# Optimization experiments

Hardware: AMD Instinct MI355X
Metric: run time of the kernel (lower is better)

Reference implementation:

```python
import jax, jax.numpy as jnp
import numpy as np
from jax import lax

INPUT = 99
HIDDEN = 64
T = 65536


def setup_inputs() -> dict:
    key = jax.random.key(0)
    ks = jax.random.split(key, 8)
    x = jax.random.normal(ks[0], (1, T, INPUT), dtype=jnp.float32)
    # PyTorch LSTM params: weight_ih_l0 [4H, in], weight_hh_l0 [4H, H], biases [4H]
    s = 1.0 / np.sqrt(HIDDEN)
    W_ih = jax.random.uniform(ks[1], (4 * HIDDEN, INPUT), jnp.float32, -s, s)
    W_hh = jax.random.uniform(ks[2], (4 * HIDDEN, HIDDEN), jnp.float32, -s, s)
    b_ih = jax.random.uniform(ks[3], (4 * HIDDEN,), jnp.float32, -s, s)
    b_hh = jax.random.uniform(ks[4], (4 * HIDDEN,), jnp.float32, -s, s)
    # head: Linear(64->32, bias=False), Linear(32->3, bias=True)
    W1 = jax.random.normal(ks[5], (32, HIDDEN), dtype=jnp.float32) * 0.01
    W2 = jax.random.normal(ks[6], (3, 32), dtype=jnp.float32) * 0.01
    b2 = jnp.zeros((3,), dtype=jnp.float32)
    return {"x": x, "W_ih": W_ih, "W_hh": W_hh, "b_ih": b_ih, "b_hh": b_hh,
            "W1": W1, "W2": W2, "b2": b2}


def reference(x, W_ih, W_hh, b_ih, b_hh, W1, W2, b2):
    H = HIDDEN
    # Precompute input projections for all timesteps (one big GEMM).
    # x: [1, T, 99] -> xz: [T, 4H]; x[-1] == last (only) batch row.
    xz = jnp.einsum('td,gd->tg', x[-1], W_ih) + b_ih + b_hh

    def step(carry, z_t):
        h, c = carry
        z = z_t + W_hh @ h  # [4H]
        i, f, g, o = jnp.split(z, 4)  # PyTorch gate order: i, f, g, o
        i = jax.nn.sigmoid(i)
        f = jax.nn.sigmoid(f)
        g = jnp.tanh(g)
        o = jax.nn.sigmoid(o)
        c = f * c + i * g
        h = o * jnp.tanh(c)
        return (h, c), None

    h0 = jnp.zeros((H,), dtype=x.dtype)
    c0 = jnp.zeros((H,), dtype=x.dtype)
    (h_T, _), _ = lax.scan(step, (h0, c0), xz)

    # x[-1, -1] -> last timestep hidden of last batch row, then MLP head
    h = jax.nn.relu(h_T)
    h = jax.nn.relu(W1 @ h)
    out = W2 @ h + b2
    return out[None, :]  # [1, 3]
```

## Files before the change

kernel.cpp:

```cpp
#include <hip/hip_runtime.h>

#define T_STEPS 65536
#define NIN 99
#define HID 64
#define G4 256
#define TS 128
#define PF 8

typedef _Float16 half2v __attribute__((ext_vector_type(2)));

__device__ __forceinline__ float frcp(float x) { return __builtin_amdgcn_rcpf(x); }
__device__ __forceinline__ float fexp2(float x) { return __builtin_amdgcn_exp2f(x); }

#define LOG2E 1.4426950408889634f

__device__ __forceinline__ float sigmoid_f(float x) { return frcp(1.0f + fexp2(x * -LOG2E)); }
__device__ __forceinline__ float tanh_f(float x) {
    float ax = fabsf(x);
    float e  = fexp2(ax * (2.0f * LOG2E));
    float r  = 1.0f - 2.0f * frcp(e + 1.0f);
    return copysignf(r, x);
}

__device__ __forceinline__ half2v pk16(float a, float b) {
#if __has_builtin(__builtin_amdgcn_cvt_pkrtz)
    return __builtin_bit_cast(half2v, __builtin_amdgcn_cvt_pkrtz(a, b));
#else
    half2v r; r.x = (_Float16)a; r.y = (_Float16)b; return r;
#endif
}
__device__ __forceinline__ float fdot2f(half2v a, half2v b, float c) {
#if __has_builtin(__builtin_amdgcn_fdot2)
    return __builtin_amdgcn_fdot2(a, b, c, false);
#else
    return fmaf((float)a.x, (float)b.x, fmaf((float)a.y, (float)b.y, c));
#endif
}

#define BAR_LGKM() asm volatile("s_waitcnt lgkmcnt(0)\n\ts_barrier" ::: "memory")

__global__ __launch_bounds__(256, 1) void xz_kernel(
    const float* __restrict__ x, const float* __restrict__ W_ih,
    const float* __restrict__ b_ih, const float* __restrict__ b_hh,
    float* __restrict__ xz2) {
    __shared__ __align__(16) float xs[TS * 100];
    const int g  = threadIdx.x;
    const int t0 = blockIdx.x * TS;
    const int unit = g & 63, d = g >> 6;

    for (int i = g; i < TS * NIN; i += 256) {
        int tl = i / NIN;
        int j  = i - tl * NIN;
        xs[tl * 100 + j] = x[(size_t)t0 * NIN + i];
    }

    float w[NIN];
#pragma unroll
    for (int j = 0; j < NIN; ++j) w[j] = W_ih[g * NIN + j];
    const float bias = b_ih[g] + b_hh[g];
    __syncthreads();

    for (int tl = 0; tl < TS; ++tl) {
        const float* xr = &xs[tl * 100];
        float a0 = bias, a1 = 0.f, a2 = 0.f, a3 = 0.f;
#pragma unroll
        for (int j4 = 0; j4 < 24; ++j4) {
            float4 xv = *(const float4*)(xr + 4 * j4);
            a0 = fmaf(w[4 * j4 + 0], xv.x, a0);
            a1 = fmaf(w[4 * j4 + 1], xv.y, a1);
            a2 = fmaf(w[4 * j4 + 2], xv.z, a2);
            a3 = fmaf(w[4 * j4 + 3], xv.w, a3);
        }
        a0 = fmaf(w[96], xr[96], a0);
        a1 = fmaf(w[97], xr[97], a1);
        a2 = fmaf(w[98], xr[98], a2);
        xz2[(size_t)(t0 + tl) * G4 + unit * 4 + d] = (a0 + a1) + (a2 + a3);
    }
}

__global__ __launch_bounds__(256, 1) __attribute__((amdgpu_waves_per_eu(1)))
void lstm_kernel(
    const float* __restrict__ xz2, const float* __restrict__ W_hh,
    const float* __restrict__ W1, const float* __restrict__ W2,
    const float* __restrict__ b2, float* __restrict__ out) {
    __shared__ __align__(16) float4 pbuf[2][4][HID];
    __shared__ float hfin[HID];
    __shared__ float hbuf[32];
    const int tid = threadIdx.x;
    const int l   = tid & 63;
    const int wv  = tid >> 6;
    const int sb  = __builtin_amdgcn_readfirstlane(16 * wv);

    const float* Wb = W_hh + l * HID + sb;
    int wiP[8], wfP[8], wgP[8], woP[8];
#pragma unroll
    for (int j = 0; j < 8; ++j) {
        wiP[j] = __builtin_bit_cast(int, pk16(Wb[2 * j + 0],     Wb[2 * j + 1]));
        wfP[j] = __builtin_bit_cast(int, pk16(Wb[2 * j + 4096],  Wb[2 * j + 4097]));
        wgP[j] = __builtin_bit_cast(int, pk16(Wb[2 * j + 8192],  Wb[2 * j + 8193]));
        woP[j] = __builtin_bit_cast(int, pk16(Wb[2 * j + 12288], Wb[2 * j + 12289]));
        asm volatile("" : "+v"(wiP[j]), "+v"(wfP[j]), "+v"(wgP[j]), "+v"(woP[j]));
    }

    float h = 0.0f, c = 0.0f;

    const float* zi = xz2 + 4 * l;
    float4 zc0 = *(const float4*)(zi + (size_t)(wv)     * G4);
    float4 zc1 = *(const float4*)(zi + (size_t)(wv + 4) * G4);
    float4 zn0 = make_float4(0.f, 0.f, 0.f, 0.f);
    float4 zn1 = make_float4(0.f, 0.f, 0.f, 0.f);

    for (int tb = 0; tb < T_STEPS; tb += PF) {
        if (tb + PF < T_STEPS) {
            zn0 = *(const float4*)(zi + (size_t)(tb + PF + wv)     * G4);
            zn1 = *(const float4*)(zi + (size_t)(tb + PF + wv + 4) * G4);
        }
#pragma unroll
        for (int u = 0; u < PF; ++u) {
            const int par = u & 1;
            float ai, af, ag, ao;
            if (wv == (u & 3)) {
                float4 z = (u < 4) ? zc0 : zc1;
                ai = z.x; af = z.y; ag = z.z; ao = z.w;
            } else { ai = 0.f; af = 0.f; ag = 0.f; ao = 0.f; }

#if __has_builtin(__builtin_amdgcn_mov_dpp)
            float hn = __int_as_float(__builtin_amdgcn_mov_dpp(
                __float_as_int(h), 0xB1 , 0xF, 0xF, true));
#else
            float hn = __shfl_xor(h, 1, 64);
#endif
            const int hpi = __builtin_bit_cast(int, pk16(h, hn));
#pragma unroll
            for (int j = 0; j < 8; ++j) {
                half2v hpj = __builtin_bit_cast(half2v,
                    __builtin_amdgcn_readlane(hpi, sb + 2 * j));
                ai = fdot2f(__builtin_bit_cast(half2v, wiP[j]), hpj, ai);
                af = fdot2f(__builtin_bit_cast(half2v, wfP[j]), hpj, af);
                ag = fdot2f(__builtin_bit_cast(half2v, wgP[j]), hpj, ag);
                ao = fdot2f(__builtin_bit_cast(half2v, woP[j]), hpj, ao);
            }
            pbuf[par][wv][l] = make_float4(ai, af, ag, ao);
            BAR_LGKM();

            float4 r0 = pbuf[par][(wv + 1) & 3][l];
            float4 r1 = pbuf[par][(wv + 2) & 3][l];
            float4 r2 = pbuf[par][(wv + 3) & 3][l];
            float si = (ai + r0.x) + (r1.x + r2.x);
            float sf = (af + r0.y) + (r1.y + r2.y);
            float sg = (ag + r0.z) + (r1.z + r2.z);
            float so = (ao + r0.w) + (r1.w + r2.w);
            float ig = sigmoid_f(si);
            float fg = sigmoid_f(sf);
            float gg = tanh_f(sg);
            float og = sigmoid_f(so);
            c = fmaf(fg, c, ig * gg);
            h = og * tanh_f(c);
        }
        zc0 = zn0; zc1 = zn1;
    }

    if (tid < HID) hfin[tid] = h;
    __syncthreads();
    if (tid < 32) {
        float s = 0.0f;
#pragma unroll
        for (int j = 0; j < HID; ++j) s += W1[tid * HID + j] * fmaxf(hfin[j], 0.0f);
        hbuf[tid] = fmaxf(s, 0.0f);
    }
    __syncthreads();
    if (tid < 3) {
        float s = b2[tid];
#pragma unroll
        for (int j = 0; j < 32; ++j) s += W2[tid * 32 + j] * hbuf[j];
        out[tid] = s;
    }
}

extern "C" void kernel_launch(void* const* d_in, const int* in_sizes, int n_in,
                              void* d_out, int out_size, void* d_ws, size_t ws_size,
                              hipStream_t stream) {
    const float* x   = (const float*)d_in[0];
    const float* Wih = (const float*)d_in[1];
    const float* Whh = (const float*)d_in[2];
    const float* bih = (const float*)d_in[3];
    const float* bhh = (const float*)d_in[4];
    const float* W1  = (const float*)d_in[5];
    const float* W2  = (const float*)d_in[6];
    const float* b2  = (const float*)d_in[7];
    float* out = (float*)d_out;
    float* xz2 = (float*)d_ws;

    xz_kernel<<<T_STEPS / TS, 256, 0, stream>>>(x, Wih, bih, bhh, xz2);
    lstm_kernel<<<1, 256, 0, stream>>>(xz2, Whh, W1, W2, b2, out);
}
```

Measured before the change: 23.37 ms.

## Run LSTM recurrence in a single wavefront, removing LDS reduction and barriers

```diff
diff --git a/kernel.cpp b/kernel.cpp
--- a/kernel.cpp
+++ b/kernel.cpp
@@ -5,7 +5,7 @@
 #define HID 64
 #define G4 256
 #define TS 128
-#define PF 8
+#define PF 4
 
 typedef _Float16 half2v __attribute__((ext_vector_type(2)));
 
@@ -36,8 +36,6 @@
     return fmaf((float)a.x, (float)b.x, fmaf((float)a.y, (float)b.y, c));
 #endif
 }
-
-#define BAR_LGKM() asm volatile("s_waitcnt lgkmcnt(0)\n\ts_barrier" ::: "memory")
 
 __global__ __launch_bounds__(256, 1) void xz_kernel(
     const float* __restrict__ x, const float* __restrict__ W_ih,
@@ -78,23 +76,19 @@
     }
 }
 
-__global__ __launch_bounds__(256, 1) __attribute__((amdgpu_waves_per_eu(1)))
+__global__ __launch_bounds__(64, 1) __attribute__((amdgpu_waves_per_eu(1)))
 void lstm_kernel(
     const float* __restrict__ xz2, const float* __restrict__ W_hh,
     const float* __restrict__ W1, const float* __restrict__ W2,
     const float* __restrict__ b2, float* __restrict__ out) {
-    __shared__ __align__(16) float4 pbuf[2][4][HID];
     __shared__ float hfin[HID];
     __shared__ float hbuf[32];
-    const int tid = threadIdx.x;
-    const int l   = tid & 63;
-    const int wv  = tid >> 6;
-    const int sb  = __builtin_amdgcn_readfirstlane(16 * wv);
+    const int l = threadIdx.x;
 
-    const float* Wb = W_hh + l * HID + sb;
-    int wiP[8], wfP[8], wgP[8], woP[8];
+    const float* Wb = W_hh + l * HID;
+    int wiP[32], wfP[32], wgP[32], woP[32];
 #pragma unroll
-    for (int j = 0; j < 8; ++j) {
+    for (int j = 0; j < 32; ++j) {
         wiP[j] = __builtin_bit_cast(int, pk16(Wb[2 * j + 0],     Wb[2 * j + 1]));
         wfP[j] = __builtin_bit_cast(int, pk16(Wb[2 * j + 4096],  Wb[2 * j + 4097]));
         wgP[j] = __builtin_bit_cast(int, pk16(Wb[2 * j + 8192],  Wb[2 * j + 8193]));
@@ -105,24 +99,21 @@
     float h = 0.0f, c = 0.0f;
 
     const float* zi = xz2 + 4 * l;
-    float4 zc0 = *(const float4*)(zi + (size_t)(wv)     * G4);
-    float4 zc1 = *(const float4*)(zi + (size_t)(wv + 4) * G4);
-    float4 zn0 = make_float4(0.f, 0.f, 0.f, 0.f);
-    float4 zn1 = make_float4(0.f, 0.f, 0.f, 0.f);
+    float4 zcur[PF], znxt[PF];
+#pragma unroll
+    for (int p = 0; p < PF; ++p) zcur[p] = *(const float4*)(zi + (size_t)p * G4);
 
     for (int tb = 0; tb < T_STEPS; tb += PF) {
         if (tb + PF < T_STEPS) {
-            zn0 = *(const float4*)(zi + (size_t)(tb + PF + wv)     * G4);
-            zn1 = *(const float4*)(zi + (size_t)(tb + PF + wv + 4) * G4);
+#pragma unroll
+            for (int p = 0; p < PF; ++p)
+                znxt[p] = *(const float4*)(zi + (size_t)(tb + PF + p) * G4);
         }
 #pragma unroll
         for (int u = 0; u < PF; ++u) {
-            const int par = u & 1;
-            float ai, af, ag, ao;
-            if (wv == (u & 3)) {
-                float4 z = (u < 4) ? zc0 : zc1;
-                ai = z.x; af = z.y; ag = z.z; ao = z.w;
-            } else { ai = 0.f; af = 0.f; ag = 0.f; ao = 0.f; }
+            const float4 z = zcur[u];
+            float ai0 = z.x, af0 = z.y, ag0 = z.z, ao0 = z.w;
+            float ai1 = 0.f, af1 = 0.f, ag1 = 0.f, ao1 = 0.f;
 
 #if __has_builtin(__builtin_amdgcn_mov_dpp)
             float hn = __int_as_float(__builtin_amdgcn_mov_dpp(
@@ -132,24 +123,24 @@
 #endif
             const int hpi = __builtin_bit_cast(int, pk16(h, hn));
 #pragma unroll
-            for (int j = 0; j < 8; ++j) {
-                half2v hpj = __builtin_bit_cast(half2v,
-                    __builtin_amdgcn_readlane(hpi, sb + 2 * j));
-                ai = fdot2f(__builtin_bit_cast(half2v, wiP[j]), hpj, ai);
-                af = fdot2f(__builtin_bit_cast(half2v, wfP[j]), hpj, af);
-                ag = fdot2f(__builtin_bit_cast(half2v, wgP[j]), hpj, ag);
-                ao = fdot2f(__builtin_bit_cast(half2v, woP[j]), hpj, ao);
+            for (int j = 0; j < 16; ++j) {
+                half2v hp0 = __builtin_bit_cast(half2v,
+                    __builtin_amdgcn_readlane(hpi, 4 * j + 0));
+                half2v hp1 = __builtin_bit_cast(half2v,
+                    __builtin_amdgcn_readlane(hpi, 4 * j + 2));
+                ai0 = fdot2f(__builtin_bit_cast(half2v, wiP[2 * j]),     hp0, ai0);
+                af0 = fdot2f(__builtin_bit_cast(half2v, wfP[2 * j]),     hp0, af0);
+                ag0 = fdot2f(__builtin_bit_cast(half2v, wgP[2 * j]),     hp0, ag0);
+                ao0 = fdot2f(__builtin_bit_cast(half2v, woP[2 * j]),     hp0, ao0);
+                ai1 = fdot2f(__builtin_bit_cast(half2v, wiP[2 * j + 1]), hp1, ai1);
+                af1 = fdot2f(__builtin_bit_cast(half2v, wfP[2 * j + 1]), hp1, af1);
+                ag1 = fdot2f(__builtin_bit_cast(half2v, wgP[2 * j + 1]), hp1, ag1);
+                ao1 = fdot2f(__builtin_bit_cast(half2v, woP[2 * j + 1]), hp1, ao1);
             }
-            pbuf[par][wv][l] = make_float4(ai, af, ag, ao);
-            BAR_LGKM();
-
-            float4 r0 = pbuf[par][(wv + 1) & 3][l];
-            float4 r1 = pbuf[par][(wv + 2) & 3][l];
-            float4 r2 = pbuf[par][(wv + 3) & 3][l];
-            float si = (ai + r0.x) + (r1.x + r2.x);
-            float sf = (af + r0.y) + (r1.y + r2.y);
-            float sg = (ag + r0.z) + (r1.z + r2.z);
-            float so = (ao + r0.w) + (r1.w + r2.w);
+            float si = ai0 + ai1;
+            float sf = af0 + af1;
+            float sg = ag0 + ag1;
+            float so = ao0 + ao1;
             float ig = sigmoid_f(si);
             float fg = sigmoid_f(sf);
             float gg = tanh_f(sg);
@@ -157,23 +148,24 @@
             c = fmaf(fg, c, ig * gg);
             h = og * tanh_f(c);
         }
-        zc0 = zn0; zc1 = zn1;
+#pragma unroll
+        for (int p = 0; p < PF; ++p) zcur[p] = znxt[p];
     }
 
-    if (tid < HID) hfin[tid] = h;
+    hfin[l] = h;
     __syncthreads();
-    if (tid < 32) {
+    if (l < 32) {
         float s = 0.0f;
 #pragma unroll
-        for (int j = 0; j < HID; ++j) s += W1[tid * HID + j] * fmaxf(hfin[j], 0.0f);
-        hbuf[tid] = fmaxf(s, 0.0f);
+        for (int j = 0; j < HID; ++j) s += W1[l * HID + j] * fmaxf(hfin[j], 0.0f);
+        hbuf[l] = fmaxf(s, 0.0f);
     }
     __syncthreads();
-    if (tid < 3) {
-        float s = b2[tid];
+    if (l < 3) {
+        float s = b2[l];
 #pragma unroll
-        for (int j = 0; j < 32; ++j) s += W2[tid * 32 + j] * hbuf[j];
-        out[tid] = s;
+        for (int j = 0; j < 32; ++j) s += W2[l * 32 + j] * hbuf[j];
+        out[l] = s;
     }
 }
 
@@ -192,5 +184,5 @@
     float* xz2 = (float*)d_ws;
 
     xz_kernel<<<T_STEPS / TS, 256, 0, stream>>>(x, Wih, bih, bhh, xz2);
-    lstm_kernel<<<1, 256, 0, stream>>>(xz2, Whh, W1, W2, b2, out);
+    lstm_kernel<<<1, 64, 0, stream>>>(xz2, Whh, W1, W2, b2, out);
 }
```

Result: slower. 29.05 ms (+24.3%).
